# Kernel optimization log

Measured on AMD Instinct MI355X. Metric: run time of the kernel, lower is better.

Reference implementation:

```python
import jax, jax.numpy as jnp
import numpy as np

MAXV = 127.0  # 2**(8-1) - 1, signed int8 symmetric range


def setup_inputs() -> dict:
    key = jax.random.key(0)
    kx, kw, kb = jax.random.split(key, 3)
    x = jax.random.normal(kx, (4, 2048, 4096), dtype=jnp.float32)
    weight = jax.random.normal(kw, (4096, 4096), dtype=jnp.float32) * 0.02
    bias = jax.random.normal(kb, (4096,), dtype=jnp.float32) * 0.01
    return {"x": x, "weight": weight, "bias": bias}


def reference(x, weight, bias):
    # Per-tensor max calibration (TensorQuantizer.amax)
    amax_x = jnp.max(jnp.abs(x))
    amax_w = jnp.max(jnp.abs(weight))
    sx = MAXV / amax_x
    sw = MAXV / amax_w
    # Quantize to int8 (fake_quant=False path -> integer tensors)
    qx = jnp.clip(jnp.round(x * sx), -MAXV, MAXV).astype(jnp.int8)
    qw = jnp.clip(jnp.round(weight * sw), -MAXV, MAXV).astype(jnp.int8)
    # Exact systolic int8 MAC -> int32 accumulate: [b, s, out]
    out_i32 = jnp.matmul(
        qx.astype(jnp.int32), qw.astype(jnp.int32).T,
        preferred_element_type=jnp.int32,
    )
    # Dequantize and add bias
    out = out_i32.astype(jnp.float32) / (sx * sw) + bias
    return out
```

## Files before the change

### kernel.cpp

```cpp
#include <hip/hip_runtime.h>

#define MAXV 127.0f
#define Mdim 8192
#define Ndim 4096
#define Kdim 4096

#define EW_GRID 2048
#define EW_BLOCK 256
#define EW_STRIDE (EW_GRID * EW_BLOCK)

typedef __attribute__((ext_vector_type(4))) int int32x4;

__device__ __forceinline__ void async_load16(const void* g, void* l) {
  __builtin_amdgcn_global_load_lds(
      (const __attribute__((address_space(1))) unsigned int*)g,
      (__attribute__((address_space(3))) unsigned int*)l, 16, 0, 0);
}

__device__ __forceinline__ float amax4(float4 v) {
  return fmaxf(fmaxf(fabsf(v.x), fabsf(v.y)), fmaxf(fabsf(v.z), fabsf(v.w)));
}

__global__ __launch_bounds__(EW_BLOCK) void amax_both_kernel(
    const float4* __restrict__ x, const float4* __restrict__ w,
    int* __restrict__ out_bits) {
  const int t = blockIdx.x * EW_BLOCK + threadIdx.x;
  float mx = 0.0f, mw = 0.0f;
#pragma unroll
  for (int i = 0; i < 4; i++) {
    float4 a = x[t + (4 * i + 0) * EW_STRIDE];
    float4 b = x[t + (4 * i + 1) * EW_STRIDE];
    float4 c = x[t + (4 * i + 2) * EW_STRIDE];
    float4 d = x[t + (4 * i + 3) * EW_STRIDE];
    mx = fmaxf(mx, fmaxf(fmaxf(amax4(a), amax4(b)), fmaxf(amax4(c), amax4(d))));
  }
#pragma unroll
  for (int i = 0; i < 2; i++) {
    float4 a = w[t + (4 * i + 0) * EW_STRIDE];
    float4 b = w[t + (4 * i + 1) * EW_STRIDE];
    float4 c = w[t + (4 * i + 2) * EW_STRIDE];
    float4 d = w[t + (4 * i + 3) * EW_STRIDE];
    mw = fmaxf(mw, fmaxf(fmaxf(amax4(a), amax4(b)), fmaxf(amax4(c), amax4(d))));
  }
  for (int off = 32; off > 0; off >>= 1) {
    mx = fmaxf(mx, __shfl_down(mx, off));
    mw = fmaxf(mw, __shfl_down(mw, off));
  }
  __shared__ float sm[8];
  if ((threadIdx.x & 63) == 0) {
    sm[threadIdx.x >> 6] = mx;
    sm[4 + (threadIdx.x >> 6)] = mw;
  }
  __syncthreads();
  if (threadIdx.x == 0) {
    atomicMax(out_bits,
              __float_as_int(fmaxf(fmaxf(sm[0], sm[1]), fmaxf(sm[2], sm[3]))));
    atomicMax(out_bits + 1,
              __float_as_int(fmaxf(fmaxf(sm[4], sm[5]), fmaxf(sm[6], sm[7]))));
  }
}

__device__ __forceinline__ char4 quant4(float4 v, float s) {
  char4 q;
  q.x = (signed char)(int)fminf(fmaxf(rintf(v.x * s), -MAXV), MAXV);
  q.y = (signed char)(int)fminf(fmaxf(rintf(v.y * s), -MAXV), MAXV);
  q.z = (signed char)(int)fminf(fmaxf(rintf(v.z * s), -MAXV), MAXV);
  q.w = (signed char)(int)fminf(fmaxf(rintf(v.w * s), -MAXV), MAXV);
  return q;
}

__global__ __launch_bounds__(EW_BLOCK) void quant_both_kernel(
    const float4* __restrict__ x, const float4* __restrict__ w,
    const int* __restrict__ amax_bits, char4* __restrict__ qx,
    char4* __restrict__ qw) {
  const float sx = MAXV / __int_as_float(amax_bits[0]);
  const float sw = MAXV / __int_as_float(amax_bits[1]);
  const int t = blockIdx.x * EW_BLOCK + threadIdx.x;
#pragma unroll
  for (int i = 0; i < 4; i++) {
    int i0 = t + (4 * i + 0) * EW_STRIDE, i1 = t + (4 * i + 1) * EW_STRIDE;
    int i2 = t + (4 * i + 2) * EW_STRIDE, i3 = t + (4 * i + 3) * EW_STRIDE;
    float4 a = x[i0], b = x[i1], c = x[i2], d = x[i3];
    qx[i0] = quant4(a, sx);
    qx[i1] = quant4(b, sx);
    qx[i2] = quant4(c, sx);
    qx[i3] = quant4(d, sx);
  }
#pragma unroll
  for (int i = 0; i < 2; i++) {
    int i0 = t + (4 * i + 0) * EW_STRIDE, i1 = t + (4 * i + 1) * EW_STRIDE;
    int i2 = t + (4 * i + 2) * EW_STRIDE, i3 = t + (4 * i + 3) * EW_STRIDE;
    float4 a = w[i0], b = w[i1], c = w[i2], d = w[i3];
    qw[i0] = quant4(a, sw);
    qw[i1] = quant4(b, sw);
    qw[i2] = quant4(c, sw);
    qw[i3] = quant4(d, sw);
  }
}

#define BM 256
#define BN 256
#define BKB 128
#define HALF 16384
#define NIT 15

#define LDSA(buf) (lds + ((buf) * 4 + wm) * HALF)
#define LDSB(buf) (lds + ((buf) * 4 + 2 + (wn >> 1)) * HALF)

#define STG_A(buf, h, kt)                                          \
  {                                                                \
    signed char* d = lds + ((buf) * 4 + (h)) * HALF + wdst;        \
    const signed char* s = aS + (h) * HSK + (size_t)(kt) * BKB;    \
    async_load16(s, d);                                            \
    async_load16(s + 64 * (size_t)Kdim, d + 8192);                 \
  }
#define STG_B(buf, h, kt)                                          \
  {                                                                \
    signed char* d = lds + ((buf) * 4 + 2 + (h)) * HALF + wdst;    \
    const signed char* s = bS + (h) * HSK + (size_t)(kt) * BKB;    \
    async_load16(s, d);                                            \
    async_load16(s + 64 * (size_t)Kdim, d + 8192);                 \
  }

#define LOAD_A(buf, mh)                                            \
  {                                                                \
    const signed char* ab = LDSA(buf) + (mh) * 8192;               \
    _Pragma("unroll") for (int mi = 0; mi < 4; mi++) {             \
      afr[mi][0] = *(const int32x4*)(ab + mi * 2048 + aoff0);      \
      afr[mi][1] = *(const int32x4*)(ab + mi * 2048 + aoff1);      \
    }                                                              \
  }
#define LOAD_B(buf, g)                                             \
  {                                                                \
    const signed char* bb = LDSB(buf) + brow0 + (g) * 4096;        \
    _Pragma("unroll") for (int j = 0; j < 2; j++) {                \
      bfr[(g) * 2 + j][0] = *(const int32x4*)(bb + j * 2048 + aoff0); \
      bfr[(g) * 2 + j][1] = *(const int32x4*)(bb + j * 2048 + aoff1); \
    }                                                              \
  }

#define MFMA_Q(ma, nb)                                                        \
  _Pragma("unroll") for (int mi = 0; mi < 4; mi++)                            \
  _Pragma("unroll") for (int nj = 0; nj < 2; nj++)                            \
  _Pragma("unroll") for (int ks = 0; ks < 2; ks++)                            \
      acc[(ma) * 4 + mi][(nb) * 2 + nj] =                                     \
          __builtin_amdgcn_mfma_i32_16x16x64_i8(                              \
              afr[mi][ks], bfr[(nb) * 2 + nj][ks],                            \
              acc[(ma) * 4 + mi][(nb) * 2 + nj], 0, 0, 0);

#define SYNC_MID()                                       \
  __builtin_amdgcn_s_barrier();                          \
  asm volatile("s_waitcnt lgkmcnt(0)" ::: "memory");     \
  __builtin_amdgcn_sched_barrier(0);                     \
  __builtin_amdgcn_s_setprio(1);

#define PH_END()                \
  __builtin_amdgcn_s_setprio(0); \
  __builtin_amdgcn_s_barrier();

#define PH_END_V(n)                                      \
  __builtin_amdgcn_s_setprio(0);                         \
  asm volatile("s_waitcnt vmcnt(" #n ")" ::: "memory");  \
  __builtin_amdgcn_s_barrier();

__global__ __launch_bounds__(512, 2) void gemm_i8_kernel(
    const signed char* __restrict__ Aq, const signed char* __restrict__ Bq,
    const float* __restrict__ bias, const int* __restrict__ amax_bits,
    float* __restrict__ out) {
  __shared__ signed char lds[8 * HALF];

  const int tid = threadIdx.x;
  const int lane = tid & 63;
  const int w = tid >> 6;
  const int wm = w >> 2;
  const int wn = w & 3;

  const int m0 = blockIdx.y * BM;
  const int n0 = blockIdx.x * BN;

  const int r0 = tid >> 3;
  const int gcol = ((tid & 7) * 16) ^ ((r0 & 7) << 4);
  const signed char* aS = Aq + (size_t)(m0 + r0) * Kdim + gcol;
  const signed char* bS = Bq + (size_t)(n0 + r0) * Kdim + gcol;
  const size_t HSK = (size_t)128 * Kdim;
  const int wdst = w * 1024;

  const int aoff0 =
      (lane & 15) * 128 + (((lane >> 4) * 16) ^ ((lane & 7) << 4));
  const int aoff1 =
      (lane & 15) * 128 + ((64 + (lane >> 4) * 16) ^ ((lane & 7) << 4));
  const int brow0 = (wn & 1) * 8192;

  int32x4 acc[8][4] = {};
  int32x4 afr[4][2], bfr[4][2];

  STG_A(0, 0, 0);
  STG_A(0, 1, 0);
  STG_B(0, 0, 0);
  STG_B(0, 1, 0);
  STG_B(1, 0, 1);
  STG_B(1, 1, 1);
  asm volatile("s_waitcnt vmcnt(4)" ::: "memory");
  __builtin_amdgcn_s_barrier();

#pragma unroll 1
  for (int it = 0; it < NIT; ++it) {
    const int kt1 = 2 * it + 1, kt2 = 2 * it + 2, kt3 = 2 * it + 3;
    LOAD_A(0, 0); LOAD_B(0, 0); STG_A(1, 0, kt1);
    SYNC_MID(); MFMA_Q(0, 0); PH_END();
    LOAD_B(0, 1); STG_A(1, 1, kt1);
    SYNC_MID(); MFMA_Q(0, 1); PH_END();
    LOAD_A(0, 1); STG_B(0, 0, kt2);
    SYNC_MID(); MFMA_Q(1, 1); PH_END();
    STG_B(0, 1, kt2);
    SYNC_MID(); MFMA_Q(1, 0); PH_END_V(4);
    LOAD_A(1, 0); LOAD_B(1, 0); STG_A(0, 0, kt2);
    SYNC_MID(); MFMA_Q(0, 0); PH_END();
    LOAD_B(1, 1); STG_A(0, 1, kt2);
    SYNC_MID(); MFMA_Q(0, 1); PH_END();
    LOAD_A(1, 1); STG_B(1, 0, kt3);
    SYNC_MID(); MFMA_Q(1, 1); PH_END();
    STG_B(1, 1, kt3);
    SYNC_MID(); MFMA_Q(1, 0); PH_END_V(4);
  }

  {
    LOAD_A(0, 0); LOAD_B(0, 0); STG_A(1, 0, 31);
    SYNC_MID(); MFMA_Q(0, 0); PH_END();
    LOAD_B(0, 1); STG_A(1, 1, 31);
    SYNC_MID(); MFMA_Q(0, 1); PH_END();
    LOAD_A(0, 1);
    SYNC_MID(); MFMA_Q(1, 1); PH_END();
    SYNC_MID(); MFMA_Q(1, 0); PH_END_V(0);
    LOAD_A(1, 0); LOAD_B(1, 0);
    SYNC_MID(); MFMA_Q(0, 0); PH_END();
    LOAD_B(1, 1);
    SYNC_MID(); MFMA_Q(0, 1); PH_END();
    LOAD_A(1, 1);
    SYNC_MID(); MFMA_Q(1, 1); PH_END();
    SYNC_MID(); MFMA_Q(1, 0);
    __builtin_amdgcn_s_setprio(0);
  }

  const float sx = MAXV / __int_as_float(amax_bits[0]);
  const float sw = MAXV / __int_as_float(amax_bits[1]);
  const float inv = 1.0f / (sx * sw);
  const int crow = (lane >> 4) * 4;
  const int ccol = lane & 15;
#pragma unroll
  for (int nj = 0; nj < 4; nj++) {
    const int n = n0 + wn * 64 + nj * 16 + ccol;
    const float bv = bias[n];
#pragma unroll
    for (int a = 0; a < 8; a++) {
      const int m = m0 + wm * 128 + a * 16 + crow;
      float* op = out + (size_t)m * Ndim + n;
#pragma unroll
      for (int r = 0; r < 4; r++)
        op[(size_t)r * Ndim] = (float)acc[a][nj][r] * inv + bv;
    }
  }
}

extern "C" void kernel_launch(void* const* d_in, const int* in_sizes, int n_in,
                              void* d_out, int out_size, void* d_ws,
                              size_t ws_size, hipStream_t stream) {
  const float* x = (const float*)d_in[0];
  const float* wgt = (const float*)d_in[1];
  const float* bias = (const float*)d_in[2];
  float* out = (float*)d_out;

  int* amax = (int*)d_ws;
  signed char* qx = (signed char*)d_ws + 256;
  signed char* qw = qx + (size_t)Mdim * Kdim;

  hipMemsetAsync(amax, 0, 2 * sizeof(int), stream);
  hipLaunchKernelGGL(amax_both_kernel, dim3(EW_GRID), dim3(EW_BLOCK), 0, stream,
                     (const float4*)x, (const float4*)wgt, amax);
  hipLaunchKernelGGL(quant_both_kernel, dim3(EW_GRID), dim3(EW_BLOCK), 0,
                     stream, (const float4*)x, (const float4*)wgt, amax,
                     (char4*)qx, (char4*)qw);
  hipLaunchKernelGGL(gemm_i8_kernel, dim3(Ndim / BN, Mdim / BM), dim3(512), 0,
                     stream, qx, qw, bias, amax, out);
}
```

Baseline: 430.0 us.

## Fuse amax and quantize into one cooperative kernel with grid sync

Replaces the separate amax and quantize launches with one cooperative kernel. Each thread reduces the max over its chunk of x and w, the blocks meet at a grid-wide sync, and then the same threads quantize to int8 with wide 16-byte stores. If the cooperative launch fails it falls back to the old two-kernel path. It also drops the lgkmcnt wait and sched_barrier from the GEMM mid-phase sync, which risks a race on LDS fragment reads.

```diff
diff --git a/kernel.cpp b/kernel.cpp
--- a/kernel.cpp
+++ b/kernel.cpp
@@ -1,4 +1,5 @@
 #include <hip/hip_runtime.h>
+#include <hip/hip_cooperative_groups.h>
 
 #define MAXV 127.0f
 #define Mdim 8192
@@ -8,6 +9,10 @@
 #define EW_GRID 2048
 #define EW_BLOCK 256
 #define EW_STRIDE (EW_GRID * EW_BLOCK)
+#define FEW_GRID 1024
+#define FEW_THREADS (FEW_GRID * 256)
+#define XG4 (Mdim * Kdim / 16)
+#define WG4 (Ndim * Kdim / 16)
 
 typedef __attribute__((ext_vector_type(4))) int int32x4;
 
@@ -19,6 +24,75 @@
 
 __device__ __forceinline__ float amax4(float4 v) {
   return fmaxf(fmaxf(fabsf(v.x), fabsf(v.y)), fmaxf(fabsf(v.z), fabsf(v.w)));
+}
+
+__device__ __forceinline__ int pack4(float4 v, float s) {
+  int a = (int)fminf(fmaxf(rintf(v.x * s), -MAXV), MAXV);
+  int b = (int)fminf(fmaxf(rintf(v.y * s), -MAXV), MAXV);
+  int c = (int)fminf(fmaxf(rintf(v.z * s), -MAXV), MAXV);
+  int d = (int)fminf(fmaxf(rintf(v.w * s), -MAXV), MAXV);
+  return (a & 255) | ((b & 255) << 8) | ((c & 255) << 16) | (d << 24);
+}
+
+__global__ __launch_bounds__(256) void fused_ew_kernel(
+    const float4* __restrict__ x, const float4* __restrict__ w,
+    int* __restrict__ amax_bits, int32x4* __restrict__ qx,
+    int32x4* __restrict__ qw) {
+  const int t = blockIdx.x * 256 + threadIdx.x;
+  float mx = 0.0f, mw = 0.0f;
+#pragma unroll 2
+  for (int r = 0; r < 8; r++) {
+    const float4* p = x + 4 * ((size_t)r * FEW_THREADS + t);
+    float4 a = p[0], b = p[1], c = p[2], d = p[3];
+    mx = fmaxf(mx, fmaxf(fmaxf(amax4(a), amax4(b)), fmaxf(amax4(c), amax4(d))));
+  }
+#pragma unroll 2
+  for (int r = 0; r < 4; r++) {
+    const float4* p = w + 4 * ((size_t)r * FEW_THREADS + t);
+    float4 a = p[0], b = p[1], c = p[2], d = p[3];
+    mw = fmaxf(mw, fmaxf(fmaxf(amax4(a), amax4(b)), fmaxf(amax4(c), amax4(d))));
+  }
+  for (int off = 32; off > 0; off >>= 1) {
+    mx = fmaxf(mx, __shfl_down(mx, off));
+    mw = fmaxf(mw, __shfl_down(mw, off));
+  }
+  __shared__ float sm[8];
+  if ((threadIdx.x & 63) == 0) {
+    sm[threadIdx.x >> 6] = mx;
+    sm[4 + (threadIdx.x >> 6)] = mw;
+  }
+  __syncthreads();
+  if (threadIdx.x == 0) {
+    atomicMax(amax_bits,
+              __float_as_int(fmaxf(fmaxf(sm[0], sm[1]), fmaxf(sm[2], sm[3]))));
+    atomicMax(amax_bits + 1,
+              __float_as_int(fmaxf(fmaxf(sm[4], sm[5]), fmaxf(sm[6], sm[7]))));
+  }
+  cooperative_groups::this_grid().sync();
+  const float sx = MAXV / __int_as_float(amax_bits[0]);
+  const float sw = MAXV / __int_as_float(amax_bits[1]);
+#pragma unroll 2
+  for (int r = 0; r < 8; r++) {
+    const size_t g = (size_t)r * FEW_THREADS + t;
+    const float4* p = x + 4 * g;
+    int32x4 q;
+    q[0] = pack4(p[0], sx);
+    q[1] = pack4(p[1], sx);
+    q[2] = pack4(p[2], sx);
+    q[3] = pack4(p[3], sx);
+    qx[g] = q;
+  }
+#pragma unroll 2
+  for (int r = 0; r < 4; r++) {
+    const size_t g = (size_t)r * FEW_THREADS + t;
+    const float4* p = w + 4 * g;
+    int32x4 q;
+    q[0] = pack4(p[0], sw);
+    q[1] = pack4(p[1], sw);
+    q[2] = pack4(p[2], sw);
+    q[3] = pack4(p[3], sw);
+    qw[g] = q;
+  }
 }
 
 __global__ __launch_bounds__(EW_BLOCK) void amax_both_kernel(
@@ -148,10 +222,8 @@
               afr[mi][ks], bfr[(nb) * 2 + nj][ks],                            \
               acc[(ma) * 4 + mi][(nb) * 2 + nj], 0, 0, 0);
 
-#define SYNC_MID()                                       \
-  __builtin_amdgcn_s_barrier();                          \
-  asm volatile("s_waitcnt lgkmcnt(0)" ::: "memory");     \
-  __builtin_amdgcn_sched_barrier(0);                     \
+#define SYNC_MID()              \
+  __builtin_amdgcn_s_barrier(); \
   __builtin_amdgcn_s_setprio(1);
 
 #define PH_END()                \
@@ -275,11 +347,23 @@
   signed char* qw = qx + (size_t)Mdim * Kdim;
 
   hipMemsetAsync(amax, 0, 2 * sizeof(int), stream);
-  hipLaunchKernelGGL(amax_both_kernel, dim3(EW_GRID), dim3(EW_BLOCK), 0, stream,
-                     (const float4*)x, (const float4*)wgt, amax);
-  hipLaunchKernelGGL(quant_both_kernel, dim3(EW_GRID), dim3(EW_BLOCK), 0,
-                     stream, (const float4*)x, (const float4*)wgt, amax,
-                     (char4*)qx, (char4*)qw);
+
+  const float4* xp = (const float4*)x;
+  const float4* wp = (const float4*)wgt;
+  int* ap = amax;
+  int32x4* qx4 = (int32x4*)qx;
+  int32x4* qw4 = (int32x4*)qw;
+  void* args[5] = {&xp, &wp, &ap, &qx4, &qw4};
+  hipError_t ce = hipLaunchCooperativeKernel(
+      (const void*)fused_ew_kernel, dim3(FEW_GRID), dim3(256), args, 0, stream);
+  if (ce != hipSuccess) {
+    hipLaunchKernelGGL(amax_both_kernel, dim3(EW_GRID), dim3(EW_BLOCK), 0,
+                       stream, (const float4*)x, (const float4*)wgt, amax);
+    hipLaunchKernelGGL(quant_both_kernel, dim3(EW_GRID), dim3(EW_BLOCK), 0,
+                       stream, (const float4*)x, (const float4*)wgt, amax,
+                       (char4*)qx, (char4*)qw);
+  }
+
   hipLaunchKernelGGL(gemm_i8_kernel, dim3(Ndim / BN, Mdim / BM), dim3(512), 0,
                      stream, qx, qw, bias, amax, out);
 }
```

New measurement: 547.5 us. 27.3% more time.
